# Kernel optimization log

Measured on AMD Instinct MI355X. Metric: run time of the kernel, lower is better.

Reference implementation:

```python
import jax, jax.numpy as jnp
import numpy as np

N, K, DIM, A, M = 20000, 16, 256, 128, 2500
EPS = 1e-5
SCALE = float(np.sqrt(A))


def _ln(x, g, b):
    mu = x.mean(-1, keepdims=True)
    var = x.var(-1, keepdims=True)
    return (x - mu) / jnp.sqrt(var + EPS) * g + b


def _pe(x, w1, b1, w2, b2):
    # PositionEncoder: Linear -> ReLU -> Linear
    return jax.nn.relu(x @ w1 + b1) @ w2 + b2


def setup_inputs() -> dict:
    key = jax.random.key(0)
    ks = jax.random.split(key, 24)
    w = lambda k, s, fan: jax.random.normal(k, s, jnp.float32) / np.sqrt(fan)
    inp = {
        'events': jax.random.normal(ks[0], (N, 4), jnp.float32),
        'features': jax.random.normal(ks[1], (N, DIM), jnp.float32),
        'local_idx': jax.random.randint(ks[2], (N, K), 0, N, jnp.int32),
        'down_idx': jax.random.randint(ks[3], (M,), 0, N, jnp.int32),
        'pair_idx': jax.random.randint(ks[4], (M, K), 0, N, jnp.int32),
        'inv_pair_idx': jax.random.randint(ks[5], (N, K), 0, M, jnp.int32),
        'local_qkv_w': w(ks[6], (DIM, 3 * A), DIM), 'local_qkv_b': jnp.zeros((3 * A,), jnp.float32),
        'local_pe_w1': w(ks[7], (4, A), 4), 'local_pe_b1': jnp.zeros((A,), jnp.float32),
        'local_pe_w2': w(ks[8], (A, A), A), 'local_pe_b2': jnp.zeros((A,), jnp.float32),
        'local_fc_g': jnp.ones((A,), jnp.float32), 'local_fc_b': jnp.zeros((A,), jnp.float32),
        'global_qkv_w': w(ks[9], (DIM, 3 * A), DIM), 'global_qkv_b': jnp.zeros((3 * A,), jnp.float32),
        'global_pe_w1': w(ks[10], (4, A), 4), 'global_pe_b1': jnp.zeros((A,), jnp.float32),
        'global_pe_w2': w(ks[11], (A, A), A), 'global_pe_b2': jnp.zeros((A,), jnp.float32),
        'global_fc_g': jnp.ones((A,), jnp.float32), 'global_fc_b': jnp.zeros((A,), jnp.float32),
        'proj_w1': w(ks[12], (2 * A, DIM), 2 * A), 'proj_b1': jnp.zeros((DIM,), jnp.float32),
        'proj_w2': w(ks[13], (DIM, DIM), DIM), 'proj_b2': jnp.zeros((DIM,), jnp.float32),
    }
    return inp


def _local_attn(events, features, local_idx, qkv_w, qkv_b,
                pe_w1, pe_b1, pe_w2, pe_b2, fc_g, fc_b):
    # pos enc on event-coordinate differences to the 16 knn neighbors
    pe = _pe(events[:, None, :] - events[local_idx], pe_w1, pe_b1, pe_w2, pe_b2)  # [N,K,A]
    qkv = features @ qkv_w + qkv_b
    q, k, v = jnp.split(qkv, 3, axis=-1)               # [N,A] each
    kg, vg = k[local_idx], v[local_idx]                # [N,K,A]
    attn = _ln(q[:, None, :] - kg + pe, fc_g, fc_b) / SCALE
    attn = jax.nn.softmax(attn, axis=1)                # softmax over neighbors
    return jnp.sum(attn * (vg + pe), axis=1)           # [N,A]


def _global_attn(events, features, down_idx, pair_idx, inv_pair_idx,
                 qkv_w, qkv_b, pe_w1, pe_b1, pe_w2, pe_b2, fc_g, fc_b):
    down_events = events[down_idx]                     # [M,4]
    pe = _pe(events[:, None, :] - down_events[inv_pair_idx], pe_w1, pe_b1, pe_w2, pe_b2)  # [N,K,A]
    qkv = features @ qkv_w + qkv_b
    q, k, v = jnp.split(qkv, 3, axis=-1)
    kmax = jnp.max(k[pair_idx], axis=1)                # [M,A] pooled over k support pts
    vmax = jnp.max(v[pair_idx], axis=1)
    kg, vg = kmax[inv_pair_idx], vmax[inv_pair_idx]    # [N,K,A]
    attn = _ln(q[:, None, :] - kg + pe, fc_g, fc_b) / SCALE
    attn = jax.nn.softmax(attn, axis=1)
    return jnp.sum(attn * (vg + pe), axis=1)


def reference(events, features, local_idx, down_idx, pair_idx, inv_pair_idx,
              local_qkv_w, local_qkv_b, local_pe_w1, local_pe_b1, local_pe_w2, local_pe_b2,
              local_fc_g, local_fc_b,
              global_qkv_w, global_qkv_b, global_pe_w1, global_pe_b1, global_pe_w2, global_pe_b2,
              global_fc_g, global_fc_b,
              proj_w1, proj_b1, proj_w2, proj_b2):
    la = _local_attn(events, features, local_idx, local_qkv_w, local_qkv_b,
                     local_pe_w1, local_pe_b1, local_pe_w2, local_pe_b2,
                     local_fc_g, local_fc_b)
    ga = _global_attn(events, features, down_idx, pair_idx, inv_pair_idx,
                      global_qkv_w, global_qkv_b, global_pe_w1, global_pe_b1,
                      global_pe_w2, global_pe_b2, global_fc_g, global_fc_b)
    attn = jnp.concatenate([la, ga], axis=-1)          # [N,2A]
    # proj MLP: Linear -> ReLU -> Linear
    return jax.nn.relu(attn @ proj_w1 + proj_b1) @ proj_w2 + proj_b2
```

## Files before the change

kernel.cpp:

```cpp
#include <hip/hip_runtime.h>

#define N_PTS 20000
#define KNN   16
#define DIMF  256
#define AD    128
#define MD    2500
#define EPSV  1e-5f
#define INV_SCALE 0.08838834764831845f
#define NEG_BIG -3.402823466e38f

typedef __attribute__((ext_vector_type(8))) short short8v;
typedef __attribute__((ext_vector_type(4))) float f32x4;

__device__ __forceinline__ float b2f(unsigned short u) {
  union { unsigned int i; float f; } v; v.i = ((unsigned int)u) << 16; return v.f;
}
__device__ __forceinline__ unsigned short f2b(float f) {
  union { float f; unsigned int i; } v; v.f = f;
  unsigned int x = v.i;
  return (unsigned short)((x + 0x7fffu + ((x >> 16) & 1u)) >> 16);
}

__global__ void EventAttention_54382875902362_kernel(float* out) {
  if (threadIdx.x == 0 && blockIdx.x == 0) out[0] = 8192.0f;
}

__global__ void prep_w2(const float* __restrict__ w2l, const float* __restrict__ w2g,
                        unsigned short* __restrict__ w2B)
{
  int id  = blockIdx.x * 256 + threadIdx.x;
  int br  = id >> 14;
  int rem = id & 16383;
  int e  = rem & 7;
  int l  = (rem >> 3) & 63;
  int ks = (rem >> 9) & 3;
  int tt = rem >> 11;
  int n = tt * 16 + (l & 15);
  int i = ks * 32 + (l >> 4) * 8 + e;
  const float* src = br ? w2g : w2l;
  w2B[id] = f2b(src[i * AD + n]);
}

__global__ void prep_frag(const float* __restrict__ src, unsigned short* __restrict__ dst,
                          int ncols, int frag_elems)
{
  int id = blockIdx.x * 256 + threadIdx.x;
  if (id >= frag_elems) return;
  int e  = id & 7;
  int l  = (id >> 3) & 63;
  int ks = (id >> 9) & 7;
  int tt = id >> 12;
  int n = tt * 16 + (l & 15);
  int k = ks * 32 + (l >> 4) * 8 + e;
  float v = src[k * ncols + n];
  unsigned short hi = f2b(v);
  unsigned short lo = f2b(v - b2f(hi));
  dst[id] = hi;
  dst[frag_elems + id] = lo;
}

__global__ void qkv_mfma(const float* __restrict__ feat,
                         const unsigned short* __restrict__ wfl, const float* __restrict__ bl,
                         const unsigned short* __restrict__ wfg, const float* __restrict__ bg,
                         float* __restrict__ qkv_l, float* __restrict__ qkv_g)
{
  __shared__ __align__(16) unsigned short aHi[16 * 256];
  __shared__ __align__(16) unsigned short aLo[16 * 256];
  const int tid  = threadIdx.x;
  const int lane = tid & 63;
  const int wv   = tid >> 6;
  const int br   = blockIdx.x & 1;
  const int row0 = (blockIdx.x >> 1) * 16;

  {
    int r = tid >> 4, seg = tid & 15;
    const float4* src = (const float4*)(feat + (size_t)(row0 + r) * 256 + seg * 16);
    #pragma unroll
    for (int q4 = 0; q4 < 4; ++q4) {
      float4 f = src[q4];
      int byte = (r * 512 + (seg * 16 + q4 * 4) * 2) ^ ((r & 7) << 4);
      ushort4 h, l2;
      h.x = f2b(f.x); l2.x = f2b(f.x - b2f(h.x));
      h.y = f2b(f.y); l2.y = f2b(f.y - b2f(h.y));
      h.z = f2b(f.z); l2.z = f2b(f.z - b2f(h.z));
      h.w = f2b(f.w); l2.w = f2b(f.w - b2f(h.w));
      *(ushort4*)((char*)aHi + byte) = h;
      *(ushort4*)((char*)aLo + byte) = l2;
    }
  }
  __syncthreads();

  short8v ah[8], al[8];
  #pragma unroll
  for (int ks = 0; ks < 8; ++ks) {
    int base = ((lane & 15) * 512 + ks * 64 + (lane >> 4) * 16) ^ ((lane & 7) << 4);
    ah[ks] = *(const short8v*)((const char*)aHi + base);
    al[ks] = *(const short8v*)((const char*)aLo + base);
  }
  const unsigned short* wf = br ? wfg : wfl;
  const float* bias        = br ? bg : bl;
  float* outp              = br ? qkv_g : qkv_l;
  const short8v* wH = (const short8v*)wf;
  const short8v* wL = wH + 12288;
  f32x4 acc[6];
  #pragma unroll
  for (int t = 0; t < 6; ++t) acc[t] = (f32x4){0.f, 0.f, 0.f, 0.f};
  #pragma unroll
  for (int t = 0; t < 6; ++t) {
    int tt = wv * 6 + t;
    #pragma unroll
    for (int ks = 0; ks < 8; ++ks) {
      short8v bh = wH[(tt * 8 + ks) * 64 + lane];
      short8v bo = wL[(tt * 8 + ks) * 64 + lane];
      acc[t] = __builtin_amdgcn_mfma_f32_16x16x32_bf16(ah[ks], bh, acc[t], 0, 0, 0);
      acc[t] = __builtin_amdgcn_mfma_f32_16x16x32_bf16(al[ks], bh, acc[t], 0, 0, 0);
      acc[t] = __builtin_amdgcn_mfma_f32_16x16x32_bf16(ah[ks], bo, acc[t], 0, 0, 0);
    }
  }
  #pragma unroll
  for (int t = 0; t < 6; ++t) {
    int colb = (wv * 6 + t) * 16 + (lane & 15);
    float bv = bias[colb];
    #pragma unroll
    for (int r = 0; r < 4; ++r) {
      int row = (lane >> 4) * 4 + r;
      outp[(size_t)(row0 + row) * 384 + colb] = acc[t][r] + bv;
    }
  }
}

__global__ void kvmax_kernel(const float* __restrict__ qkv_g,
                             const int* __restrict__ pair_idx,
                             float* __restrict__ kmax, float* __restrict__ vmax)
{
  const int m = blockIdx.x, a = threadIdx.x;
  float km = NEG_BIG, vm = NEG_BIG;
  for (int j = 0; j < KNN; ++j) {
    int p = pair_idx[m * KNN + j];
    km = fmaxf(km, qkv_g[(size_t)p * 384 + 128 + a]);
    vm = fmaxf(vm, qkv_g[(size_t)p * 384 + 256 + a]);
  }
  kmax[m * AD + a] = km;
  vmax[m * AD + a] = vm;
}

__global__ void attn_fused(const float* __restrict__ events,
                           const int* __restrict__ local_idx,
                           const int* __restrict__ inv_pair_idx,
                           const int* __restrict__ down_idx,
                           const float* __restrict__ qkv_l,
                           const float* __restrict__ qkv_g,
                           const float* __restrict__ kmax,
                           const float* __restrict__ vmax,
                           const float* __restrict__ w1L, const float* __restrict__ b1L,
                           const unsigned short* __restrict__ w2BL, const float* __restrict__ b2L,
                           const float* __restrict__ gL,  const float* __restrict__ bbL,
                           const float* __restrict__ w1G, const float* __restrict__ b1G,
                           const unsigned short* __restrict__ w2BG, const float* __restrict__ b2G,
                           const float* __restrict__ gG,  const float* __restrict__ bbG,
                           float* __restrict__ out)
{
  __shared__ __align__(16) unsigned short hB[KNN * AD];
  __shared__ float scratch[KNN * 132];
  __shared__ float dS[KNN][4];
  __shared__ float red[2][KNN][2];

  const int bid  = blockIdx.x;
  const int gbr  = bid & 1;
  const int n    = bid >> 1;
  const int a    = threadIdx.x;
  const int lane = a & 63;
  const int wv   = a >> 6;

  const int*   idx = gbr ? inv_pair_idx : local_idx;
  const float* qt  = gbr ? qkv_g : qkv_l;
  const float* kt  = gbr ? kmax : (qkv_l + 128);
  const float* vt  = gbr ? vmax : (qkv_l + 256);
  const int    ks_ = gbr ? 128 : 384;
  const float* w1  = gbr ? w1G : w1L;
  const float* b1  = gbr ? b1G : b1L;
  const unsigned short* w2B = gbr ? w2BG : w2BL;
  const float* b2  = gbr ? b2G : b2L;
  const float* gg  = gbr ? gG : gL;
  const float* bbp = gbr ? bbG : bbL;

  int id[KNN];
  #pragma unroll
  for (int j = 0; j < KNN; ++j) id[j] = idx[n * KNN + j];

  const float qv = qt[(size_t)n * 384 + a];
  float kg[KNN], vg[KNN];
  #pragma unroll
  for (int j = 0; j < KNN; ++j) kg[j] = kt[(size_t)id[j] * ks_ + a];
  #pragma unroll
  for (int j = 0; j < KNN; ++j) vg[j] = vt[(size_t)id[j] * ks_ + a];

  if (a < KNN * 4) {
    int j = a >> 2, c = a & 3;
    int erow = gbr ? down_idx[id[j]] : id[j];
    dS[j][c] = events[(size_t)n * 4 + c] - events[(size_t)erow * 4 + c];
  }
  const float w1r0 = w1[0 * AD + a];
  const float w1r1 = w1[1 * AD + a];
  const float w1r2 = w1[2 * AD + a];
  const float w1r3 = w1[3 * AD + a];
  const float b1r = b1[a];
  const float b2r = b2[a];
  const float gr  = gg[a] * INV_SCALE;
  const float brv = bbp[a] * INV_SCALE;
  __syncthreads();

  #pragma unroll
  for (int j = 0; j < KNN; ++j) {
    const float4 d = *(const float4*)dS[j];
    float h = b1r;
    h = fmaf(d.x, w1r0, h);
    h = fmaf(d.y, w1r1, h);
    h = fmaf(d.z, w1r2, h);
    h = fmaf(d.w, w1r3, h);
    h = fmaxf(h, 0.f);
    int byte = (j * 256 + a * 2) ^ ((j & 7) << 4);
    *(unsigned short*)((char*)hB + byte) = f2b(h);
  }
  __syncthreads();

  short8v af[4];
  #pragma unroll
  for (int ksl = 0; ksl < 4; ++ksl) {
    int base = ((lane & 15) * 256 + ksl * 64 + (lane >> 4) * 16) ^ ((lane & 7) << 4);
    af[ksl] = *(const short8v*)((const char*)hB + base);
  }
  f32x4 acc[4];
  #pragma unroll
  for (int t = 0; t < 4; ++t) acc[t] = (f32x4){0.f, 0.f, 0.f, 0.f};
  const short8v* wf = (const short8v*)w2B;
  #pragma unroll
  for (int t = 0; t < 4; ++t) {
    #pragma unroll
    for (int ksl = 0; ksl < 4; ++ksl) {
      short8v bf = wf[(((wv * 4 + t) * 4 + ksl) * 64) + lane];
      acc[t] = __builtin_amdgcn_mfma_f32_16x16x32_bf16(af[ksl], bf, acc[t], 0, 0, 0);
    }
  }
  #pragma unroll
  for (int t = 0; t < 4; ++t) {
    #pragma unroll
    for (int r = 0; r < 4; ++r) {
      int row = (lane >> 4) * 4 + r;
      int col = wv * 64 + t * 16 + (lane & 15);
      scratch[row * 132 + col] = acc[t][r];
    }
  }
  __syncthreads();

  float pe[KNN], x[KNN];
  #pragma unroll
  for (int j = 0; j < KNN; ++j) {
    pe[j] = scratch[j * 132 + a] + b2r;
    x[j]  = qv - kg[j] + pe[j];
  }
  __syncthreads();

  #pragma unroll
  for (int j = 0; j < KNN; ++j) scratch[j * 129 + a] = x[j];
  __syncthreads();

  {
    int jj = a & 15, pp = a >> 4;
    float s1 = 0.f, s2 = 0.f;
    #pragma unroll
    for (int c = 0; c < 16; ++c) {
      float v = scratch[jj * 129 + pp * 16 + c];
      s1 += v;
      s2 = fmaf(v, v, s2);
    }
    s1 += __shfl_xor(s1, 16, 64); s2 += __shfl_xor(s2, 16, 64);
    s1 += __shfl_xor(s1, 32, 64); s2 += __shfl_xor(s2, 32, 64);
    if (lane < 16) { red[wv][jj][0] = s1; red[wv][jj][1] = s2; }
  }
  __syncthreads();

  float mx = NEG_BIG;
  #pragma unroll
  for (int j = 0; j < KNN; ++j) {
    float S1 = red[0][j][0] + red[1][j][0];
    float S2 = red[0][j][1] + red[1][j][1];
    float mu  = S1 * (1.f / AD);
    float var = S2 * (1.f / AD) - mu * mu;
    float rs  = rsqrtf(var + EPSV);
    float s = fmaf((x[j] - mu) * rs, gr, brv);
    x[j] = s;
    mx = fmaxf(mx, s);
  }
  float sum = 0.f;
  #pragma unroll
  for (int j = 0; j < KNN; ++j) {
    float p = __expf(x[j] - mx);
    x[j] = p;
    sum += p;
  }
  const float inv = 1.f / sum;
  float o = 0.f;
  #pragma unroll
  for (int j = 0; j < KNN; ++j)
    o = fmaf(x[j], vg[j] + pe[j], o);
  out[(size_t)n * 256 + (gbr ? 128 : 0) + a] = o * inv;
}

__global__ void proj_mfma(const float* __restrict__ attn_cat,
                          const unsigned short* __restrict__ w1f, const float* __restrict__ b1,
                          const unsigned short* __restrict__ w2f, const float* __restrict__ b2,
                          float* __restrict__ outp)
{
  __shared__ __align__(16) unsigned short aHi[16 * 256];
  __shared__ __align__(16) unsigned short aLo[16 * 256];
  const int tid  = threadIdx.x;
  const int lane = tid & 63;
  const int wv   = tid >> 6;
  const int row0 = blockIdx.x * 16;

  {
    int r = tid >> 4, seg = tid & 15;
    const float4* src = (const float4*)(attn_cat + (size_t)(row0 + r) * 256 + seg * 16);
    #pragma unroll
    for (int q4 = 0; q4 < 4; ++q4) {
      float4 f = src[q4];
      int byte = (r * 512 + (seg * 16 + q4 * 4) * 2) ^ ((r & 7) << 4);
      ushort4 h, l2;
      h.x = f2b(f.x); l2.x = f2b(f.x - b2f(h.x));
      h.y = f2b(f.y); l2.y = f2b(f.y - b2f(h.y));
      h.z = f2b(f.z); l2.z = f2b(f.z - b2f(h.z));
      h.w = f2b(f.w); l2.w = f2b(f.w - b2f(h.w));
      *(ushort4*)((char*)aHi + byte) = h;
      *(ushort4*)((char*)aLo + byte) = l2;
    }
  }
  __syncthreads();

  short8v ah[8], al[8];
  #pragma unroll
  for (int ks = 0; ks < 8; ++ks) {
    int base = ((lane & 15) * 512 + ks * 64 + (lane >> 4) * 16) ^ ((lane & 7) << 4);
    ah[ks] = *(const short8v*)((const char*)aHi + base);
    al[ks] = *(const short8v*)((const char*)aLo + base);
  }
  __syncthreads();

  const short8v* w1H = (const short8v*)w1f;
  const short8v* w1L = w1H + 8192;
  f32x4 acc[4];
  #pragma unroll
  for (int t = 0; t < 4; ++t) acc[t] = (f32x4){0.f, 0.f, 0.f, 0.f};
  #pragma unroll
  for (int t = 0; t < 4; ++t) {
    int tt = wv * 4 + t;
    #pragma unroll
    for (int ks = 0; ks < 8; ++ks) {
      short8v bh = w1H[(tt * 8 + ks) * 64 + lane];
      short8v bo = w1L[(tt * 8 + ks) * 64 + lane];
      acc[t] = __builtin_amdgcn_mfma_f32_16x16x32_bf16(ah[ks], bh, acc[t], 0, 0, 0);
      acc[t] = __builtin_amdgcn_mfma_f32_16x16x32_bf16(al[ks], bh, acc[t], 0, 0, 0);
      acc[t] = __builtin_amdgcn_mfma_f32_16x16x32_bf16(ah[ks], bo, acc[t], 0, 0, 0);
    }
  }
  #pragma unroll
  for (int t = 0; t < 4; ++t) {
    int col = (wv * 4 + t) * 16 + (lane & 15);
    float bvv = b1[col];
    #pragma unroll
    for (int r = 0; r < 4; ++r) {
      int row = (lane >> 4) * 4 + r;
      float h = fmaxf(acc[t][r] + bvv, 0.f);
      unsigned short hi = f2b(h);
      unsigned short lo = f2b(h - b2f(hi));
      int byte = (row * 512 + col * 2) ^ ((row & 7) << 4);
      *(unsigned short*)((char*)aHi + byte) = hi;
      *(unsigned short*)((char*)aLo + byte) = lo;
    }
  }
  __syncthreads();

  #pragma unroll
  for (int ks = 0; ks < 8; ++ks) {
    int base = ((lane & 15) * 512 + ks * 64 + (lane >> 4) * 16) ^ ((lane & 7) << 4);
    ah[ks] = *(const short8v*)((const char*)aHi + base);
    al[ks] = *(const short8v*)((const char*)aLo + base);
  }
  const short8v* w2H = (const short8v*)w2f;
  const short8v* w2L = w2H + 8192;
  #pragma unroll
  for (int t = 0; t < 4; ++t) acc[t] = (f32x4){0.f, 0.f, 0.f, 0.f};
  #pragma unroll
  for (int t = 0; t < 4; ++t) {
    int tt = wv * 4 + t;
    #pragma unroll
    for (int ks = 0; ks < 8; ++ks) {
      short8v bh = w2H[(tt * 8 + ks) * 64 + lane];
      short8v bo = w2L[(tt * 8 + ks) * 64 + lane];
      acc[t] = __builtin_amdgcn_mfma_f32_16x16x32_bf16(ah[ks], bh, acc[t], 0, 0, 0);
      acc[t] = __builtin_amdgcn_mfma_f32_16x16x32_bf16(al[ks], bh, acc[t], 0, 0, 0);
      acc[t] = __builtin_amdgcn_mfma_f32_16x16x32_bf16(ah[ks], bo, acc[t], 0, 0, 0);
    }
  }
  #pragma unroll
  for (int t = 0; t < 4; ++t) {
    int col = (wv * 4 + t) * 16 + (lane & 15);
    float bvv = b2[col];
    #pragma unroll
    for (int r = 0; r < 4; ++r) {
      int row = (lane >> 4) * 4 + r;
      outp[(size_t)(row0 + row) * 256 + col] = acc[t][r] + bvv;
    }
  }
}

extern "C" void kernel_launch(void* const* d_in, const int* in_sizes, int n_in,
                              void* d_out, int out_size, void* d_ws, size_t ws_size,
                              hipStream_t stream)
{
  const float* events   = (const float*)d_in[0];
  const float* features = (const float*)d_in[1];
  const int* local_idx    = (const int*)d_in[2];
  const int* down_idx     = (const int*)d_in[3];
  const int* pair_idx     = (const int*)d_in[4];
  const int* inv_pair_idx = (const int*)d_in[5];
  const float* l_qkv_w = (const float*)d_in[6];
  const float* l_qkv_b = (const float*)d_in[7];
  const float* l_pe_w1 = (const float*)d_in[8];
  const float* l_pe_b1 = (const float*)d_in[9];
  const float* l_pe_w2 = (const float*)d_in[10];
  const float* l_pe_b2 = (const float*)d_in[11];
  const float* l_fc_g  = (const float*)d_in[12];
  const float* l_fc_b  = (const float*)d_in[13];
  const float* g_qkv_w = (const float*)d_in[14];
  const float* g_qkv_b = (const float*)d_in[15];
  const float* g_pe_w1 = (const float*)d_in[16];
  const float* g_pe_b1 = (const float*)d_in[17];
  const float* g_pe_w2 = (const float*)d_in[18];
  const float* g_pe_b2 = (const float*)d_in[19];
  const float* g_fc_g  = (const float*)d_in[20];
  const float* g_fc_b  = (const float*)d_in[21];
  const float* p_w1 = (const float*)d_in[22];
  const float* p_b1 = (const float*)d_in[23];
  const float* p_w2 = (const float*)d_in[24];
  const float* p_b2 = (const float*)d_in[25];
  (void)in_sizes; (void)n_in; (void)out_size; (void)ws_size;

  char* ws = (char*)d_ws;
  size_t off = 0;
  float* qkv_l    = (float*)(ws + off); off += (size_t)N_PTS * 384 * 4;
  float* qkv_g    = (float*)(ws + off); off += (size_t)N_PTS * 384 * 4;
  float* kmax     = (float*)(ws + off); off += (size_t)MD * AD * 4;
  float* vmax     = (float*)(ws + off); off += (size_t)MD * AD * 4;
  float* attn_cat = (float*)(ws + off); off += (size_t)N_PTS * 256 * 4;
  unsigned short* w2B   = (unsigned short*)(ws + off); off += 32768 * 2;
  unsigned short* wfL   = (unsigned short*)(ws + off); off += 196608 * 2;
  unsigned short* wfG   = (unsigned short*)(ws + off); off += 196608 * 2;
  unsigned short* wp1   = (unsigned short*)(ws + off); off += 131072 * 2;
  unsigned short* wp2   = (unsigned short*)(ws + off); off += 131072 * 2;

  EventAttention_54382875902362_kernel<<<1, 64, 0, stream>>>((float*)d_out);
  prep_w2<<<128, 256, 0, stream>>>(l_pe_w2, g_pe_w2, w2B);
  prep_frag<<<384, 256, 0, stream>>>(l_qkv_w, wfL, 384, 98304);
  prep_frag<<<384, 256, 0, stream>>>(g_qkv_w, wfG, 384, 98304);
  prep_frag<<<256, 256, 0, stream>>>(p_w1, wp1, 256, 65536);
  prep_frag<<<256, 256, 0, stream>>>(p_w2, wp2, 256, 65536);

  qkv_mfma<<<2500, 256, 0, stream>>>(
      features, wfL, l_qkv_b, wfG, g_qkv_b, qkv_l, qkv_g);
  kvmax_kernel<<<MD, 128, 0, stream>>>(qkv_g, pair_idx, kmax, vmax);
  attn_fused<<<2 * N_PTS, 128, 0, stream>>>(
      events, local_idx, inv_pair_idx, down_idx,
      qkv_l, qkv_g, kmax, vmax,
      l_pe_w1, l_pe_b1, w2B, l_pe_b2, l_fc_g, l_fc_b,
      g_pe_w1, g_pe_b1, w2B + 16384, g_pe_b2, g_fc_g, g_fc_b,
      attn_cat);
  proj_mfma<<<N_PTS / 16, 256, 0, stream>>>(
      attn_cat, wp1, p_b1, wp2, p_b2, (float*)d_out);
}
```

Measured before the change: 244.7 us.

## Store gathered K/V as interleaved bf16 pairs to halve gather traffic

The QKV kernel now writes the local K and V as bf16 values interleaved into one 32-bit word per (point, channel), and kvmax packs the max-pooled global K/V the same way. The attention kernel gathers one 32-bit word per neighbor instead of two separate fp32 loads, which halves gather bandwidth and load count. The cost is precision: K and V are rounded to bf16 instead of the hi/lo split used elsewhere, and qkv_mfma now does scattered 2-byte stores.

```diff
diff --git a/kernel.cpp b/kernel.cpp
--- a/kernel.cpp
+++ b/kernel.cpp
@@ -62,7 +62,8 @@
 __global__ void qkv_mfma(const float* __restrict__ feat,
                          const unsigned short* __restrict__ wfl, const float* __restrict__ bl,
                          const unsigned short* __restrict__ wfg, const float* __restrict__ bg,
-                         float* __restrict__ qkv_l, float* __restrict__ qkv_g)
+                         float* __restrict__ qkv_l, float* __restrict__ qkv_g,
+                         unsigned short* __restrict__ kvl)
 {
   __shared__ __align__(16) unsigned short aHi[16 * 256];
   __shared__ __align__(16) unsigned short aLo[16 * 256];
@@ -99,7 +100,6 @@
   }
   const unsigned short* wf = br ? wfg : wfl;
   const float* bias        = br ? bg : bl;
-  float* outp              = br ? qkv_g : qkv_l;
   const short8v* wH = (const short8v*)wf;
   const short8v* wL = wH + 12288;
   f32x4 acc[6];
@@ -117,21 +117,41 @@
       acc[t] = __builtin_amdgcn_mfma_f32_16x16x32_bf16(ah[ks], bo, acc[t], 0, 0, 0);
     }
   }
-  #pragma unroll
-  for (int t = 0; t < 6; ++t) {
-    int colb = (wv * 6 + t) * 16 + (lane & 15);
-    float bv = bias[colb];
-    #pragma unroll
-    for (int r = 0; r < 4; ++r) {
-      int row = (lane >> 4) * 4 + r;
-      outp[(size_t)(row0 + row) * 384 + colb] = acc[t][r] + bv;
+  if (br) {
+    #pragma unroll
+    for (int t = 0; t < 6; ++t) {
+      int colb = (wv * 6 + t) * 16 + (lane & 15);
+      float bv = bias[colb];
+      #pragma unroll
+      for (int r = 0; r < 4; ++r) {
+        int row = (lane >> 4) * 4 + r;
+        qkv_g[(size_t)(row0 + row) * 384 + colb] = acc[t][r] + bv;
+      }
+    }
+  } else {
+    #pragma unroll
+    for (int t = 0; t < 6; ++t) {
+      int colb = (wv * 6 + t) * 16 + (lane & 15);
+      float bv = bias[colb];
+      #pragma unroll
+      for (int r = 0; r < 4; ++r) {
+        int row = (lane >> 4) * 4 + r;
+        float val = acc[t][r] + bv;
+        if (colb < 128) {
+          qkv_l[(size_t)(row0 + row) * 384 + colb] = val;
+        } else if (colb < 256) {
+          kvl[(size_t)(row0 + row) * 256 + 2 * (colb - 128)] = f2b(val);
+        } else {
+          kvl[(size_t)(row0 + row) * 256 + 2 * (colb - 256) + 1] = f2b(val);
+        }
+      }
     }
   }
 }
 
 __global__ void kvmax_kernel(const float* __restrict__ qkv_g,
                              const int* __restrict__ pair_idx,
-                             float* __restrict__ kmax, float* __restrict__ vmax)
+                             unsigned int* __restrict__ kvm)
 {
   const int m = blockIdx.x, a = threadIdx.x;
   float km = NEG_BIG, vm = NEG_BIG;
@@ -140,8 +160,7 @@
     km = fmaxf(km, qkv_g[(size_t)p * 384 + 128 + a]);
     vm = fmaxf(vm, qkv_g[(size_t)p * 384 + 256 + a]);
   }
-  kmax[m * AD + a] = km;
-  vmax[m * AD + a] = vm;
+  kvm[m * AD + a] = (unsigned int)f2b(km) | ((unsigned int)f2b(vm) << 16);
 }
 
 __global__ void attn_fused(const float* __restrict__ events,
@@ -150,8 +169,8 @@
                            const int* __restrict__ down_idx,
                            const float* __restrict__ qkv_l,
                            const float* __restrict__ qkv_g,
-                           const float* __restrict__ kmax,
-                           const float* __restrict__ vmax,
+                           const unsigned int* __restrict__ kvl,
+                           const unsigned int* __restrict__ kvm,
                            const float* __restrict__ w1L, const float* __restrict__ b1L,
                            const unsigned short* __restrict__ w2BL, const float* __restrict__ b2L,
                            const float* __restrict__ gL,  const float* __restrict__ bbL,
@@ -172,11 +191,9 @@
   const int lane = a & 63;
   const int wv   = a >> 6;
 
-  const int*   idx = gbr ? inv_pair_idx : local_idx;
-  const float* qt  = gbr ? qkv_g : qkv_l;
-  const float* kt  = gbr ? kmax : (qkv_l + 128);
-  const float* vt  = gbr ? vmax : (qkv_l + 256);
-  const int    ks_ = gbr ? 128 : 384;
+  const int*          idx = gbr ? inv_pair_idx : local_idx;
+  const float*        qt  = gbr ? qkv_g : qkv_l;
+  const unsigned int* kvp = gbr ? kvm : kvl;
   const float* w1  = gbr ? w1G : w1L;
   const float* b1  = gbr ? b1G : b1L;
   const unsigned short* w2B = gbr ? w2BG : w2BL;
@@ -189,11 +206,10 @@
   for (int j = 0; j < KNN; ++j) id[j] = idx[n * KNN + j];
 
   const float qv = qt[(size_t)n * 384 + a];
-  float kg[KNN], vg[KNN];
-  #pragma unroll
-  for (int j = 0; j < KNN; ++j) kg[j] = kt[(size_t)id[j] * ks_ + a];
-  #pragma unroll
-  for (int j = 0; j < KNN; ++j) vg[j] = vt[(size_t)id[j] * ks_ + a];
+  unsigned int kvw[KNN];
+  #pragma unroll
+  for (int j = 0; j < KNN; ++j) kvw[j] = kvp[(size_t)id[j] * AD + a];
+  asm volatile("" ::: "memory");
 
   if (a < KNN * 4) {
     int j = a >> 2, c = a & 3;
@@ -257,7 +273,7 @@
   #pragma unroll
   for (int j = 0; j < KNN; ++j) {
     pe[j] = scratch[j * 132 + a] + b2r;
-    x[j]  = qv - kg[j] + pe[j];
+    x[j]  = qv - b2f((unsigned short)kvw[j]) + pe[j];
   }
   __syncthreads();
 
@@ -303,7 +319,7 @@
   float o = 0.f;
   #pragma unroll
   for (int j = 0; j < KNN; ++j)
-    o = fmaf(x[j], vg[j] + pe[j], o);
+    o = fmaf(x[j], b2f((unsigned short)(kvw[j] >> 16)) + pe[j], o);
   out[(size_t)n * 256 + (gbr ? 128 : 0) + a] = o * inv;
 }
 
@@ -450,8 +466,8 @@
   size_t off = 0;
   float* qkv_l    = (float*)(ws + off); off += (size_t)N_PTS * 384 * 4;
   float* qkv_g    = (float*)(ws + off); off += (size_t)N_PTS * 384 * 4;
-  float* kmax     = (float*)(ws + off); off += (size_t)MD * AD * 4;
-  float* vmax     = (float*)(ws + off); off += (size_t)MD * AD * 4;
+  unsigned short* kvl = (unsigned short*)(ws + off); off += (size_t)N_PTS * 256 * 2;
+  unsigned int*   kvm = (unsigned int*)(ws + off);   off += (size_t)MD * AD * 4;
   float* attn_cat = (float*)(ws + off); off += (size_t)N_PTS * 256 * 4;
   unsigned short* w2B   = (unsigned short*)(ws + off); off += 32768 * 2;
   unsigned short* wfL   = (unsigned short*)(ws + off); off += 196608 * 2;
@@ -467,11 +483,11 @@
   prep_frag<<<256, 256, 0, stream>>>(p_w2, wp2, 256, 65536);
 
   qkv_mfma<<<2500, 256, 0, stream>>>(
-      features, wfL, l_qkv_b, wfG, g_qkv_b, qkv_l, qkv_g);
-  kvmax_kernel<<<MD, 128, 0, stream>>>(qkv_g, pair_idx, kmax, vmax);
+      features, wfL, l_qkv_b, wfG, g_qkv_b, qkv_l, qkv_g, kvl);
+  kvmax_kernel<<<MD, 128, 0, stream>>>(qkv_g, pair_idx, kvm);
   attn_fused<<<2 * N_PTS, 128, 0, stream>>>(
       events, local_idx, inv_pair_idx, down_idx,
-      qkv_l, qkv_g, kmax, vmax,
+      qkv_l, qkv_g, (const unsigned int*)kvl, kvm,
       l_pe_w1, l_pe_b1, w2B, l_pe_b2, l_fc_g, l_fc_b,
       g_pe_w1, g_pe_b1, w2B + 16384, g_pe_b2, g_fc_g, g_fc_b,
       attn_cat);
```

New measurement: 225.8 us. 7.7% less time.
